# Kernel tuning notes

Hardware: AMD Instinct MI355X
Metric: run time of the kernel (lower is better)

The kernel has to match this reference:

```python
import jax, jax.numpy as jnp
import numpy as np

LEVEL_SIZES = [6, 24, 96, 384, 1536, 6144]
NUM_LABELS = sum(LEVEL_SIZES)  # 8190
IN_FEATURES = 768
BATCH = 8192


def setup_inputs() -> dict:
    key = jax.random.key(0)
    ks = jax.random.split(key, 2 * len(LEVEL_SIZES) + 1)
    inp = {"x": jax.random.normal(ks[0], (BATCH, IN_FEATURES), dtype=jnp.float32)}
    layer_in = IN_FEATURES
    for i, out in enumerate(LEVEL_SIZES):
        scale = 1.0 / np.sqrt(layer_in)
        inp[f"W{i}"] = jax.random.uniform(ks[2 * i + 1], (out, layer_in), jnp.float32, -scale, scale)
        inp[f"b{i}"] = jax.random.uniform(ks[2 * i + 2], (out,), jnp.float32, -scale, scale)
        layer_in += out
    # labels_by_level: a permutation of global label ids, split by level sizes
    rng = np.random.default_rng(42)
    inp["labels"] = jnp.asarray(rng.permutation(NUM_LABELS), dtype=jnp.int64)
    return inp


def reference(x, W0, b0, W1, b1, W2, b2, W3, b3, W4, b4, W5, b5, labels):
    Ws = [W0, W1, W2, W3, W4, W5]
    bs = [b0, b1, b2, b3, b4, b5]
    logits = jnp.zeros((x.shape[0], NUM_LABELS), dtype=x.dtype)
    cur = x
    off = 0
    for W, b, sz in zip(Ws, bs, LEVEL_SIZES):
        y = cur @ W.T + b  # [B, sz]
        lab = labels[off:off + sz]  # static slice: global columns for this level
        logits = logits.at[:, lab].set(y)
        cur = jax.nn.relu(jnp.concatenate([cur, y], axis=1))
        off += sz
    return logits
```

## Files before the change

### kernel.cpp

```cpp
#include <hip/hip_runtime.h>
#include <hip/hip_bf16.h>

#define BATCH 8192
#define NUM_LABELS 8190
#define CURW 2944
#define YW   8192

typedef __attribute__((ext_vector_type(4))) float f32x4;
typedef __attribute__((ext_vector_type(8))) short bf16x8;

#define VMCNT(n) asm volatile("s_waitcnt vmcnt(" #n ")" ::: "memory")
#define BAR() do { asm volatile("" ::: "memory"); __builtin_amdgcn_s_barrier(); asm volatile("" ::: "memory"); } while (0)
#define WAITK(n) do { asm volatile("s_waitcnt lgkmcnt(" #n ")" ::: "memory"); __builtin_amdgcn_sched_barrier(0); } while (0)

__device__ __forceinline__ unsigned short f2bf(float f) {
  unsigned u = __builtin_bit_cast(unsigned, f);
  unsigned r = u + 0x7fffu + ((u >> 16) & 1u);
  return (unsigned short)(r >> 16);
}
__device__ __forceinline__ float bf2f(unsigned short b) {
  return __builtin_bit_cast(float, (unsigned)b << 16);
}
__device__ __forceinline__ void gload_lds16(const void* g, void* l) {
  __builtin_amdgcn_global_load_lds(
      (const __attribute__((address_space(1))) void*)g,
      (__attribute__((address_space(3))) void*)l,
      16, 0, 0);
}

__global__ void k_prep_x(const float* __restrict__ x,
                         unsigned short* __restrict__ xraw,
                         unsigned short* __restrict__ cur) {
  const int TX = BATCH * 768 / 4;
  int i = blockIdx.x * 256 + threadIdx.x;
  if (i < TX) {
    float4 v = ((const float4*)x)[i];
    int e = i * 4;
    int row = e / 768;
    int col = e - row * 768;
    ushort4 a, c;
    a.x = f2bf(v.x); a.y = f2bf(v.y); a.z = f2bf(v.z); a.w = f2bf(v.w);
    c.x = f2bf(fmaxf(v.x, 0.f)); c.y = f2bf(fmaxf(v.y, 0.f));
    c.z = f2bf(fmaxf(v.z, 0.f)); c.w = f2bf(fmaxf(v.w, 0.f));
    *(ushort4*)(xraw + e) = a;
    *(ushort4*)(cur + (size_t)row * CURW + col) = c;
    return;
  }
  int j = i - TX;
  const int PP = 130;
  if (j < BATCH * PP) {
    int row = j / PP, p = j - row * PP;
    int col = p < 58 ? 774 + p : (p < 98 ? 856 + (p - 58) : 992 + (p - 98));
    cur[(size_t)row * CURW + col] = 0;
  }
}

__device__ __forceinline__ int pad2real(int kp) {
  if (kp < 774)  return kp;
  if (kp < 832)  return -1;
  if (kp < 856)  return 774 + (kp - 832);
  if (kp < 896)  return -1;
  if (kp < 992)  return 798 + (kp - 896);
  if (kp < 1024) return -1;
  if (kp < 1408) return 894 + (kp - 1024);
  return 1278 + (kp - 1408);
}

template<int KPAD, int KREAL, int NREAL>
__device__ __forceinline__ void convW(int rel, const float* __restrict__ W,
                                      unsigned short* __restrict__ Wp) {
  int n = rel / KPAD, kp = rel - n * KPAD;
  int kr = pad2real(kp);
  float v = 0.f;
  if (n < NREAL && kr >= 0) v = W[(size_t)n * KREAL + kr];
  Wp[rel] = f2bf(v);
}

__global__ void k_convert_w_all(const float* __restrict__ W0, const float* __restrict__ W1,
                                const float* __restrict__ W2, const float* __restrict__ W3,
                                const float* __restrict__ W4, const float* __restrict__ W5,
                                const int* __restrict__ labels, int* __restrict__ inv,
                                unsigned short* __restrict__ wp) {
  int i = blockIdx.x * 256 + threadIdx.x;
  if (i < NUM_LABELS) inv[labels[i]] = i;
  if (i >= 20963328) return;
  if (i < 319488) {
    if (i < 98304)       convW<768, 768, 6>  (i,          W0, wp);
    else if (i < 204800) convW<832, 774, 24> (i - 98304,  W1, wp + 98304);
    else                 convW<896, 798, 96> (i - 204800, W2, wp + 204800);
  } else {
    if (i < 712704)       convW<1024, 894, 384>  (i - 319488,  W3, wp + 319488);
    else if (i < 2875392) convW<1408, 1278, 1536>(i - 712704,  W4, wp + 712704);
    else                  convW<2944, 2814, 6144>(i - 2875392, W5, wp + 2875392);
  }
}

__global__ __launch_bounds__(256, 2) void k_fused_small(
    const unsigned short* __restrict__ xraw,
    const unsigned short* __restrict__ w0p,
    const unsigned short* __restrict__ w1p,
    const unsigned short* __restrict__ w2p,
    const float* __restrict__ b0, const float* __restrict__ b1,
    const float* __restrict__ b2,
    unsigned short* __restrict__ ybuf,
    unsigned short* __restrict__ cur) {
  __shared__ __align__(16) unsigned short As[32 * 1000];
  const int tid = threadIdx.x;
  const int l = tid & 63, w = tid >> 6;
  const int l15 = l & 15, q8 = (l >> 4) * 8;
  const int row0 = blockIdx.x * 32;
  const int mi = w >> 1;
  const int nj0 = w & 1;

  {
    const int r = tid >> 3, c8 = tid & 7;
    const unsigned short* src = xraw + (size_t)(row0 + r) * 768 + c8 * 96;
    unsigned short* dst = As + r * 1000 + c8 * 96;
#pragma unroll
    for (int i = 0; i < 12; ++i)
      *(bf16x8*)(dst + i * 8) = *(const bf16x8*)(src + i * 8);
    unsigned short* dz = As + r * 1000 + 768 + c8 * 28;
    ushort4 z = {0, 0, 0, 0};
#pragma unroll
    for (int i = 0; i < 7; ++i) *(ushort4*)(dz + i * 4) = z;
  }
  __syncthreads();

  auto level = [&](int K, int ntiles, int Nr, const unsigned short* W, int ldw,
                   const float* bias, int ycol, int ccol) {
    for (int n = nj0; n < ntiles; n += 2) {
      f32x4 acc = {0.f, 0.f, 0.f, 0.f};
      const unsigned short* wrow = W + (size_t)(n * 16 + l15) * ldw + q8;
      const unsigned short* arow = As + (mi * 16 + l15) * 1000 + q8;
#pragma unroll 2
      for (int k0 = 0; k0 < K; k0 += 32) {
        bf16x8 af = *(const bf16x8*)(arow + k0);
        bf16x8 bf = *(const bf16x8*)(wrow + k0);
        acc = __builtin_amdgcn_mfma_f32_16x16x32_bf16(af, bf, acc, 0, 0, 0);
      }
      int col = n * 16 + l15;
      if (col < Nr) {
        float bv = bias[col];
#pragma unroll
        for (int j = 0; j < 4; ++j) {
          int rl = mi * 16 + (l >> 4) * 4 + j;
          float y = acc[j] + bv;
          ybuf[(size_t)(row0 + rl) * YW + ycol + col] = f2bf(y);
          As[rl * 1000 + ccol + col] = f2bf(fmaxf(y, 0.f));
        }
      }
    }
    __syncthreads();
  };

  level(768, 1, 6,  w0p, 768, b0, 0,  768);

  {
    const int r = tid >> 3, c8 = tid & 7;
    unsigned short* p = As + r * 1000 + c8 * 96;
#pragma unroll
    for (int i = 0; i < 12; ++i) {
      bf16x8 v = *(bf16x8*)(p + i * 8);
#pragma unroll
      for (int j = 0; j < 8; ++j)
        if (((unsigned short)v[j]) & 0x8000u) v[j] = 0;
      *(bf16x8*)(p + i * 8) = v;
    }
  }
  __syncthreads();

  level(832, 2, 24, w1p, 832, b1, 6,  832);
  level(896, 6, 96, w2p, 896, b2, 30, 896);

  {
    const int r = tid >> 3, c8 = tid & 7;
    const unsigned short* srcl = As + r * 1000 + 768 + c8 * 28;
    unsigned short* dstg = cur + (size_t)(row0 + r) * CURW + 768 + c8 * 28;
#pragma unroll
    for (int i = 0; i < 7; ++i)
      *(ushort4*)(dstg + i * 4) = *(const ushort4*)(srcl + i * 4);
  }
}

__global__ __launch_bounds__(256, 2) void k_gemm(
    const unsigned short* __restrict__ A, int lda,
    const unsigned short* __restrict__ B, int ldb,
    const float* __restrict__ bias,
    unsigned short* __restrict__ ybuf,
    unsigned short* __restrict__ curout,
    int K, int Nreal, int yoff, int curoff) {
  __shared__ unsigned short Asmem[128 * 64];
  __shared__ unsigned short Bsmem[128 * 64];
  const int tid = threadIdx.x;
  const int lane = tid & 63;
  const int wid = tid >> 6;
  const int wr = wid >> 1, wc = wid & 1;
  const int brow = blockIdx.x * 128;
  const int bcol = blockIdx.y * 128;

  f32x4 acc[4][4] = {};

  for (int k0 = 0; k0 < K; k0 += 64) {
#pragma unroll
    for (int p = 0; p < 4; ++p) {
      int ch = wid * 4 + p;
      int eo = ch * 512 + lane * 8;
      int r = eo >> 6;
      int col = eo & 63;
      gload_lds16(A + (size_t)(brow + r) * lda + k0 + col, Asmem + ch * 512);
      gload_lds16(B + (size_t)(bcol + r) * ldb + k0 + col, Bsmem + ch * 512);
    }
    __syncthreads();
#pragma unroll
    for (int kk = 0; kk < 2; ++kk) {
      bf16x8 af[4], bfr[4];
      int colk = kk * 32 + (lane >> 4) * 8;
#pragma unroll
      for (int m = 0; m < 4; ++m)
        af[m] = *(const bf16x8*)(Asmem + (wr * 64 + m * 16 + (lane & 15)) * 64 + colk);
#pragma unroll
      for (int n = 0; n < 4; ++n)
        bfr[n] = *(const bf16x8*)(Bsmem + (wc * 64 + n * 16 + (lane & 15)) * 64 + colk);
#pragma unroll
      for (int m = 0; m < 4; ++m)
#pragma unroll
        for (int n = 0; n < 4; ++n)
          acc[m][n] = __builtin_amdgcn_mfma_f32_16x16x32_bf16(af[m], bfr[n], acc[m][n], 0, 0, 0);
    }
    __syncthreads();
  }

#pragma unroll
  for (int n = 0; n < 4; ++n) {
    int col = bcol + wc * 64 + n * 16 + (lane & 15);
    if (col >= Nreal) continue;
    float bv = bias[col];
#pragma unroll
    for (int m = 0; m < 4; ++m) {
#pragma unroll
      for (int j = 0; j < 4; ++j) {
        int row = brow + wr * 64 + m * 16 + (lane >> 4) * 4 + j;
        float y = acc[m][n][j] + bv;
        ybuf[(size_t)row * YW + yoff + col] = f2bf(y);
        if (curout) curout[(size_t)row * CURW + curoff + col] = f2bf(fmaxf(y, 0.f));
      }
    }
  }
}

__global__ __launch_bounds__(512, 2) void k_gemm256(
    const unsigned short* __restrict__ A, int lda,
    const unsigned short* __restrict__ B, int ldb,
    const float* __restrict__ bias,
    unsigned short* __restrict__ ybuf,
    unsigned short* __restrict__ curout,
    int K, int yoff, int curoff) {
  __shared__ __align__(16) unsigned short lds[65536];
  const int tid = threadIdx.x;
  const int l = tid & 63;
  const int w = tid >> 6;
  const int wr = w >> 2;
  const int wc = w & 3;
  const int l15 = l & 15;
  const int q8 = (l >> 4) * 8;
  const int sx = (l & 7) << 3;
  const int swz = ((l & 7) ^ (l >> 3)) * 8;

  const int bid = blockIdx.x;
  const int im = (bid & 7) * 4 + ((bid >> 3) & 3);
  const int in = bid >> 5;
  const int brow = im * 256, bcol = in * 256;

  const unsigned short* gAr0 = A + (size_t)(brow + w * 8 + (l >> 3)) * lda + swz;
  const unsigned short* gAr1 = gAr0 + (size_t)64 * lda;
  const unsigned short* gAr2 = gAr0 + (size_t)128 * lda;
  const unsigned short* gAr3 = gAr0 + (size_t)192 * lda;
  const unsigned short* gBr0 = B + (size_t)(bcol + w * 8 + (l >> 3)) * ldb + swz;
  const unsigned short* gBr1 = gBr0 + (size_t)64 * ldb;
  const unsigned short* gBr2 = gBr0 + (size_t)128 * ldb;
  const unsigned short* gBr3 = gBr0 + (size_t)192 * ldb;

  unsigned short* const dA00 = lds + w * 512;
  unsigned short* const dA01 = lds + 8192 + w * 512;
  unsigned short* const dA10 = lds + 16384 + w * 512;
  unsigned short* const dA11 = lds + 24576 + w * 512;
  unsigned short* const dB00 = lds + 32768 + w * 512;
  unsigned short* const dB01 = lds + 40960 + w * 512;
  unsigned short* const dB10 = lds + 49152 + w * 512;
  unsigned short* const dB11 = lds + 57344 + w * 512;

  const int cOff0 = (q8) ^ sx;
  const int cOff1 = (32 + q8) ^ sx;
  const int brB = (wc & 1) * 64;
  const unsigned short* const aB00 = lds + wr * 8192 + l15 * 64 + cOff0;
  const unsigned short* const aB01 = lds + wr * 8192 + l15 * 64 + cOff1;
  const unsigned short* const aB10 = lds + 16384 + wr * 8192 + l15 * 64 + cOff0;
  const unsigned short* const aB11 = lds + 16384 + wr * 8192 + l15 * 64 + cOff1;
  const unsigned short* const bB00 = lds + 32768 + (wc >> 1) * 8192 + (brB + l15) * 64 + cOff0;
  const unsigned short* const bB01 = lds + 32768 + (wc >> 1) * 8192 + (brB + l15) * 64 + cOff1;
  const unsigned short* const bB10 = lds + 49152 + (wc >> 1) * 8192 + (brB + l15) * 64 + cOff0;
  const unsigned short* const bB11 = lds + 49152 + (wc >> 1) * 8192 + (brB + l15) * 64 + cOff1;

  f32x4 acc[8][4] = {};
  bf16x8 aF[2][4], bF[2][4];

  auto stage2 = [&](const unsigned short* glo, const unsigned short* ghi,
                    unsigned short* dst, int koff) {
    gload_lds16(glo + koff, dst);
    gload_lds16(ghi + koff, dst + 4096);
  };
  auto ldAh = [&](const unsigned short* lo, const unsigned short* hi, int half) {
#pragma unroll
    for (int m = 0; m < 4; ++m) {
      aF[0][m] = *(const bf16x8*)(lo + (half * 64 + m * 16) * 64);
      aF[1][m] = *(const bf16x8*)(hi + (half * 64 + m * 16) * 64);
    }
  };
  auto ldB01f = [&](const unsigned short* lo, const unsigned short* hi) {
#pragma unroll
    for (int n = 0; n < 2; ++n) {
      bF[0][n] = *(const bf16x8*)(lo + n * 16 * 64);
      bF[1][n] = *(const bf16x8*)(hi + n * 16 * 64);
    }
  };
  auto ldB23f = [&](const unsigned short* lo, const unsigned short* hi) {
#pragma unroll
    for (int n = 2; n < 4; ++n) {
      bF[0][n] = *(const bf16x8*)(lo + n * 16 * 64);
      bF[1][n] = *(const bf16x8*)(hi + n * 16 * 64);
    }
  };
  auto MM4 = [&](int m, int mbase, int nbase) {
#pragma unroll
    for (int kk = 0; kk < 2; ++kk)
#pragma unroll
      for (int n = 0; n < 2; ++n)
        acc[mbase + m][nbase + n] = __builtin_amdgcn_mfma_f32_16x16x32_bf16(
            aF[kk][m], bF[kk][nbase + n], acc[mbase + m][nbase + n], 0, 0, 0);
  };
  auto MMAblk = [&](int mbase, int nbase) {
    __builtin_amdgcn_s_setprio(1);
#pragma unroll
    for (int kk = 0; kk < 2; ++kk)
#pragma unroll
      for (int m = 0; m < 4; ++m)
#pragma unroll
        for (int n = 0; n < 2; ++n)
          acc[mbase + m][nbase + n] = __builtin_amdgcn_mfma_f32_16x16x32_bf16(
              aF[kk][m], bF[kk][nbase + n], acc[mbase + m][nbase + n], 0, 0, 0);
    __builtin_amdgcn_s_setprio(0);
  };

#define LADDER(mb, nb, w0, w1, w2, w3) do { \
    __builtin_amdgcn_s_setprio(1); \
    WAITK(w0); MM4(0, mb, nb); \
    WAITK(w1); MM4(1, mb, nb); \
    WAITK(w2); MM4(2, mb, nb); \
    WAITK(w3); MM4(3, mb, nb); \
    __builtin_amdgcn_s_setprio(0); \
  } while (0)

  const int KT = K >> 6;
  const int NT2 = KT >> 1;

  stage2(gBr0, gBr1, dB00, 0);
  stage2(gBr2, gBr3, dB01, 0);
  stage2(gAr0, gAr1, dA00, 0);
  stage2(gAr2, gAr3, dA01, 0);
  stage2(gBr0, gBr1, dB10, 64);
  stage2(gBr2, gBr3, dB11, 64);
  stage2(gAr0, gAr1, dA10, 64);
  VMCNT(6);
  BAR();
  ldB01f(bB00, bB01);

  for (int it = 0; it < NT2; ++it) {
    const bool more = (it + 1 < NT2);
    stage2(gAr2, gAr3, dA11, 64);
    ldAh(aB00, aB01, 0);
    ldB23f(bB00, bB01);
    LADDER(0, 0, 10, 8, 6, 4);
    BAR();
    MMAblk(0, 2);
    BAR();
    if (more) stage2(gBr0, gBr1, dB00, 128);
    ldAh(aB00, aB01, 1);
    LADDER(4, 0, 6, 4, 2, 0);
    BAR();
    if (more) { stage2(gBr2, gBr3, dB01, 128); stage2(gAr0, gAr1, dA00, 128); VMCNT(6); }
    else      { VMCNT(0); }
    BAR();
    ldB01f(bB10, bB11);
    MMAblk(4, 2);
    BAR();
    if (more) stage2(gAr2, gAr3, dA01, 128);
    ldAh(aB10, aB11, 0);
    ldB23f(bB10, bB11);
    LADDER(0, 0, 10, 8, 6, 4);
    BAR();
    MMAblk(0, 2);
    BAR();
    if (more) stage2(gBr0, gBr1, dB10, 192);
    ldAh(aB10, aB11, 1);
    LADDER(4, 0, 6, 4, 2, 0);
    BAR();
    if (more) { stage2(gBr2, gBr3, dB11, 192); stage2(gAr0, gAr1, dA10, 192); VMCNT(6); }
    BAR();
    if (more) ldB01f(bB00, bB01);
    MMAblk(4, 2);
    BAR();
    gAr0 += 128; gAr1 += 128; gAr2 += 128; gAr3 += 128;
    gBr0 += 128; gBr1 += 128; gBr2 += 128; gBr3 += 128;
  }
#undef LADDER

  const int j4 = (l >> 4) * 4;
  float bv[4];
#pragma unroll
  for (int n = 0; n < 4; ++n) bv[n] = bias[bcol + wc * 64 + n * 16 + l15];
#pragma unroll
  for (int m = 0; m < 8; ++m) {
    int rowb = brow + wr * 128 + m * 16 + j4;
#pragma unroll
    for (int j = 0; j < 4; ++j) {
      size_t rbase = (size_t)(rowb + j);
#pragma unroll
      for (int n = 0; n < 4; ++n) {
        int col = bcol + wc * 64 + n * 16 + l15;
        float y = acc[m][n][j] + bv[n];
        ybuf[rbase * YW + yoff + col] = f2bf(y);
        if (curout) curout[rbase * CURW + curoff + col] = f2bf(fmaxf(y, 0.f));
      }
    }
  }
}

__global__ void k_gather(const unsigned short* __restrict__ ybuf,
                         const int* __restrict__ inv,
                         float* __restrict__ out) {
  const int half = NUM_LABELS / 2;
  int i = blockIdx.x * 256 + threadIdx.x;
  if (i >= BATCH * half) return;
  int row = i / half;
  int c2 = (i - row * half) * 2;
  int2 iv = *(const int2*)(inv + c2);
  const unsigned short* yr = ybuf + (size_t)row * YW;
  float2 v;
  v.x = bf2f(yr[iv.x]);
  v.y = bf2f(yr[iv.y]);
  *(float2*)(out + (size_t)row * NUM_LABELS + c2) = v;
}

extern "C" void kernel_launch(void* const* d_in, const int* in_sizes, int n_in,
                              void* d_out, int out_size, void* d_ws, size_t ws_size,
                              hipStream_t stream) {
  const float* x = (const float*)d_in[0];
  const float* W[6];
  const float* bias[6];
  for (int i = 0; i < 6; ++i) {
    W[i] = (const float*)d_in[1 + 2 * i];
    bias[i] = (const float*)d_in[2 + 2 * i];
  }
  const int* labels = (const int*)d_in[13];
  float* out = (float*)d_out;

  char* ws = (char*)d_ws;
  unsigned short* xraw = (unsigned short*)(ws);
  unsigned short* cur  = (unsigned short*)(ws + 12582912);
  unsigned short* wp   = (unsigned short*)(ws + 60817408);
  unsigned short* ybuf = (unsigned short*)(ws + 102744064);
  int* inv             = (int*)(ws + 236961792);

  static const int Kpad[6]   = {768, 832, 896, 1024, 1408, 2944};
  static const int Nreal[6]  = {6, 24, 96, 384, 1536, 6144};
  static const int Npad[6]   = {128, 128, 128, 384, 1536, 6144};
  static const size_t woff[6] = {0, 98304, 204800, 319488, 712704, 2875392};
  static const int yoff[6]   = {0, 6, 30, 126, 510, 2046};
  static const int curoff[6] = {768, 832, 896, 1024, 1408, 0};

  {
    int tot = BATCH * 768 / 4 + BATCH * 130;
    k_prep_x<<<(tot + 255) / 256, 256, 0, stream>>>(x, xraw, cur);
  }
  k_convert_w_all<<<(20963328 + 255) / 256, 256, 0, stream>>>(
      W[0], W[1], W[2], W[3], W[4], W[5], labels, inv, wp);

  k_fused_small<<<BATCH / 32, 256, 0, stream>>>(
      xraw, wp + woff[0], wp + woff[1], wp + woff[2],
      bias[0], bias[1], bias[2], ybuf, cur);

  {
    dim3 grid(BATCH / 128, Npad[3] / 128);
    k_gemm<<<grid, 256, 0, stream>>>(cur, CURW, wp + woff[3], Kpad[3], bias[3], ybuf,
                                     cur, Kpad[3], Nreal[3], yoff[3], curoff[3]);
  }
  for (int i = 4; i < 6; ++i) {
    int nwg = (BATCH / 256) * (Npad[i] / 256);
    k_gemm256<<<nwg, 512, 0, stream>>>(cur, CURW, wp + woff[i], Kpad[i], bias[i], ybuf,
                                       (i < 5) ? cur : (unsigned short*)nullptr,
                                       Kpad[i], yoff[i], curoff[i]);
  }

  k_gather<<<(BATCH * (NUM_LABELS / 2) + 255) / 256, 256, 0, stream>>>(ybuf, inv, out);
}
```

Before: 607.2 us.

## Restructure GEMM K-loop prefetch schedule to issue full stages earlier

Reorganizes the double-buffered GEMM main loop so all four A/B half-tiles of the next stage are issued together, with a full prologue of eight loads, and the vmcnt wait moves after the second MFMA block. B-fragment loads move to the start of each half-iteration, and the LADDER macro is inlined. The intent is to give global-to-LDS loads more time in flight and to cut stalls at barriers. Loads land in buffers in a different order, so barrier correctness depends on the new wait counts.

```diff
diff --git a/kernel.cpp b/kernel.cpp
--- a/kernel.cpp
+++ b/kernel.cpp
@@ -309,25 +309,25 @@
     gload_lds16(glo + koff, dst);
     gload_lds16(ghi + koff, dst + 4096);
   };
+  auto ldB01f = [&](const unsigned short* lo, const unsigned short* hi) {
+#pragma unroll
+    for (int n = 0; n < 2; ++n) {
+      bF[0][n] = *(const bf16x8*)(lo + n * 16 * 64);
+      bF[1][n] = *(const bf16x8*)(hi + n * 16 * 64);
+    }
+  };
+  auto ldB23f = [&](const unsigned short* lo, const unsigned short* hi) {
+#pragma unroll
+    for (int n = 2; n < 4; ++n) {
+      bF[0][n] = *(const bf16x8*)(lo + n * 16 * 64);
+      bF[1][n] = *(const bf16x8*)(hi + n * 16 * 64);
+    }
+  };
   auto ldAh = [&](const unsigned short* lo, const unsigned short* hi, int half) {
 #pragma unroll
     for (int m = 0; m < 4; ++m) {
       aF[0][m] = *(const bf16x8*)(lo + (half * 64 + m * 16) * 64);
       aF[1][m] = *(const bf16x8*)(hi + (half * 64 + m * 16) * 64);
-    }
-  };
-  auto ldB01f = [&](const unsigned short* lo, const unsigned short* hi) {
-#pragma unroll
-    for (int n = 0; n < 2; ++n) {
-      bF[0][n] = *(const bf16x8*)(lo + n * 16 * 64);
-      bF[1][n] = *(const bf16x8*)(hi + n * 16 * 64);
-    }
-  };
-  auto ldB23f = [&](const unsigned short* lo, const unsigned short* hi) {
-#pragma unroll
-    for (int n = 2; n < 4; ++n) {
-      bF[0][n] = *(const bf16x8*)(lo + n * 16 * 64);
-      bF[1][n] = *(const bf16x8*)(hi + n * 16 * 64);
     }
   };
   auto MM4 = [&](int m, int mbase, int nbase) {
@@ -351,68 +351,75 @@
     __builtin_amdgcn_s_setprio(0);
   };
 
-#define LADDER(mb, nb, w0, w1, w2, w3) do { \
-    __builtin_amdgcn_s_setprio(1); \
-    WAITK(w0); MM4(0, mb, nb); \
-    WAITK(w1); MM4(1, mb, nb); \
-    WAITK(w2); MM4(2, mb, nb); \
-    WAITK(w3); MM4(3, mb, nb); \
-    __builtin_amdgcn_s_setprio(0); \
-  } while (0)
-
   const int KT = K >> 6;
   const int NT2 = KT >> 1;
 
-  stage2(gBr0, gBr1, dB00, 0);
-  stage2(gBr2, gBr3, dB01, 0);
-  stage2(gAr0, gAr1, dA00, 0);
-  stage2(gAr2, gAr3, dA01, 0);
-  stage2(gBr0, gBr1, dB10, 64);
-  stage2(gBr2, gBr3, dB11, 64);
-  stage2(gAr0, gAr1, dA10, 64);
-  VMCNT(6);
+  stage2(gBr0, gBr1, dB00, 0);  stage2(gBr2, gBr3, dB01, 0);
+  stage2(gAr0, gAr1, dA00, 0);  stage2(gAr2, gAr3, dA01, 0);
+  stage2(gBr0, gBr1, dB10, 64); stage2(gBr2, gBr3, dB11, 64);
+  stage2(gAr0, gAr1, dA10, 64); stage2(gAr2, gAr3, dA11, 64);
+  VMCNT(8);
   BAR();
-  ldB01f(bB00, bB01);
 
   for (int it = 0; it < NT2; ++it) {
     const bool more = (it + 1 < NT2);
-    stage2(gAr2, gAr3, dA11, 64);
+    ldB01f(bB00, bB01);
     ldAh(aB00, aB01, 0);
     ldB23f(bB00, bB01);
-    LADDER(0, 0, 10, 8, 6, 4);
-    BAR();
+    __builtin_amdgcn_s_setprio(1);
+    WAITK(10); MM4(0, 0, 0);
+    WAITK(8);  MM4(1, 0, 0);
+    WAITK(6);  MM4(2, 0, 0);
+    WAITK(4);  MM4(3, 0, 0);
+    __builtin_amdgcn_s_setprio(0);
+    BAR();
+    __builtin_amdgcn_s_setprio(1);
+    WAITK(0);
     MMAblk(0, 2);
     BAR();
-    if (more) stage2(gBr0, gBr1, dB00, 128);
+    if (more) { stage2(gBr0, gBr1, dB00, 128); stage2(gBr2, gBr3, dB01, 128); }
     ldAh(aB00, aB01, 1);
-    LADDER(4, 0, 6, 4, 2, 0);
-    BAR();
-    if (more) { stage2(gBr2, gBr3, dB01, 128); stage2(gAr0, gAr1, dA00, 128); VMCNT(6); }
-    else      { VMCNT(0); }
+    __builtin_amdgcn_s_setprio(1);
+    WAITK(6); MM4(0, 4, 0);
+    WAITK(4); MM4(1, 4, 0);
+    WAITK(2); MM4(2, 4, 0);
+    WAITK(0); MM4(3, 4, 0);
+    __builtin_amdgcn_s_setprio(0);
+    BAR();
+    if (more) { stage2(gAr0, gAr1, dA00, 128); stage2(gAr2, gAr3, dA01, 128); }
+    MMAblk(4, 2);
+    if (more) { VMCNT(8); } else { VMCNT(0); }
     BAR();
     ldB01f(bB10, bB11);
-    MMAblk(4, 2);
-    BAR();
-    if (more) stage2(gAr2, gAr3, dA01, 128);
     ldAh(aB10, aB11, 0);
     ldB23f(bB10, bB11);
-    LADDER(0, 0, 10, 8, 6, 4);
-    BAR();
+    __builtin_amdgcn_s_setprio(1);
+    WAITK(10); MM4(0, 0, 0);
+    WAITK(8);  MM4(1, 0, 0);
+    WAITK(6);  MM4(2, 0, 0);
+    WAITK(4);  MM4(3, 0, 0);
+    __builtin_amdgcn_s_setprio(0);
+    BAR();
+    __builtin_amdgcn_s_setprio(1);
+    WAITK(0);
     MMAblk(0, 2);
     BAR();
-    if (more) stage2(gBr0, gBr1, dB10, 192);
+    if (more) { stage2(gBr0, gBr1, dB10, 192); stage2(gBr2, gBr3, dB11, 192); }
     ldAh(aB10, aB11, 1);
-    LADDER(4, 0, 6, 4, 2, 0);
-    BAR();
-    if (more) { stage2(gBr2, gBr3, dB11, 192); stage2(gAr0, gAr1, dA10, 192); VMCNT(6); }
-    BAR();
-    if (more) ldB01f(bB00, bB01);
+    __builtin_amdgcn_s_setprio(1);
+    WAITK(6); MM4(0, 4, 0);
+    WAITK(4); MM4(1, 4, 0);
+    WAITK(2); MM4(2, 4, 0);
+    WAITK(0); MM4(3, 4, 0);
+    __builtin_amdgcn_s_setprio(0);
+    BAR();
+    if (more) { stage2(gAr0, gAr1, dA10, 192); stage2(gAr2, gAr3, dA11, 192); }
     MMAblk(4, 2);
+    if (more) { VMCNT(8); }
     BAR();
     gAr0 += 128; gAr1 += 128; gAr2 += 128; gAr3 += 128;
     gBr0 += 128; gBr1 += 128; gBr2 += 128; gBr3 += 128;
   }
-#undef LADDER
 
   const int j4 = (l >> 4) * 4;
   float bv[4];
```

New measurement: 623.9 us. +2.7%, slower.
